# Optimization experiments

Hardware: AMD Instinct MI355X
Metric: run time of the kernel (lower is better)

## Reference

```python
import jax, jax.numpy as jnp
import numpy as np

DIM = 1024
HEADS = 16
DIM_HEAD = 64
INNER = HEADS * DIM_HEAD  # 1024
SCALE = 1.0 / DIM_HEAD ** 0.5


def setup_inputs() -> dict:
    key = jax.random.key(0)
    ks = jax.random.split(key, 5)
    x = jax.random.normal(ks[0], (4, 2048, DIM), dtype=jnp.float32)
    # nn.Linear weights stored as [out, in]; we keep [in, out] for x @ W
    Wq = jax.random.normal(ks[1], (DIM, INNER), dtype=jnp.float32) * (1.0 / np.sqrt(DIM))
    Wkv = jax.random.normal(ks[2], (DIM, 2 * INNER), dtype=jnp.float32) * (1.0 / np.sqrt(DIM))
    Wo = jax.random.normal(ks[3], (INNER, DIM), dtype=jnp.float32) * (1.0 / np.sqrt(INNER))
    bo = jax.random.normal(ks[4], (DIM,), dtype=jnp.float32) * 0.01
    return {"x": x, "Wq": Wq, "Wkv": Wkv, "Wo": Wo, "bo": bo}


def reference(x, Wq, Wkv, Wo, bo):
    b, n, _ = x.shape
    q = x @ Wq                      # [b, n, inner]
    kv = x @ Wkv                    # [b, n, 2*inner]
    k, v = jnp.split(kv, 2, axis=2)
    # 'b n (h d) -> b h n d'
    q = q.reshape(b, n, HEADS, DIM_HEAD).transpose(0, 2, 1, 3)
    k = k.reshape(b, n, HEADS, DIM_HEAD).transpose(0, 2, 1, 3)
    v = v.reshape(b, n, HEADS, DIM_HEAD).transpose(0, 2, 1, 3)
    scores = jnp.einsum('bhid,bhjd->bhij', q, k) * SCALE  # [b,h,n,n]
    attn = jax.nn.softmax(scores, axis=-1)
    out = jnp.einsum('bhij,bhjd->bhid', attn, v)          # [b,h,n,d]
    out = out.transpose(0, 2, 1, 3).reshape(b, n, INNER)  # 'b h n d -> b n (h d)'
    return out @ Wo + bo
```

## Files before the change

kernel.cpp:

```cpp
#include <hip/hip_runtime.h>
#include <hip/hip_bf16.h>

typedef unsigned short u16;
typedef unsigned int u32;
typedef __attribute__((ext_vector_type(8))) short s8v;
typedef __attribute__((ext_vector_type(4))) float f4v;
typedef __attribute__((ext_vector_type(4))) unsigned short u16x4;
typedef __attribute__((ext_vector_type(4))) unsigned int u32x4;

#define MFMA16(a,b,c) __builtin_amdgcn_mfma_f32_16x16x32_bf16((a),(b),(c),0,0,0)

#define TOKENS 8192
#define SEQ    2048
#define NH     16
#define DH     64
#define DIMK   1024
#define QPRE   0.18033688f

#if defined(__has_builtin)
#if __has_builtin(__builtin_amdgcn_exp2f)
#define EXP2(x) __builtin_amdgcn_exp2f(x)
#else
#define EXP2(x) __expf((x) * 0.69314718f)
#endif
#else
#define EXP2(x) __expf((x) * 0.69314718f)
#endif

__device__ __forceinline__ u16 f2bf(float x){
  union { float f; u32 u; } v; v.f = x;
  u32 r = v.u + 0x7FFFu + ((v.u >> 16) & 1u);
  return (u16)(r >> 16);
}

__device__ __forceinline__ void gld16(const u16* g, u16* s){
  __builtin_amdgcn_global_load_lds(
      (const __attribute__((address_space(1))) unsigned int*)(const void*)g,
      (__attribute__((address_space(3))) unsigned int*)(void*)s,
      16, 0, 0);
}

__global__ __launch_bounds__(256) void k_cast(const float* __restrict__ src,
                                              u16* __restrict__ dst){
  int i = (blockIdx.x * 256 + threadIdx.x) * 4;
  float4 v = *(const float4*)(src + i);
  u16x4 vh;
  float a[4] = {v.x, v.y, v.z, v.w};
#pragma unroll
  for (int j = 0; j < 4; j++) vh[j] = f2bf(a[j]);
  *(u16x4*)(dst + i) = vh;
}

__global__ __launch_bounds__(256) void k_transpose(const float* __restrict__ s0, int c0,
                                                   const float* __restrict__ s1, int c1,
                                                   int K, u16* __restrict__ dh){
  __shared__ float tile[64][65];
  int nb = blockIdx.x * 64, kb = blockIdx.y * 64;
  int tr = threadIdx.x >> 6, tc = threadIdx.x & 63;
#pragma unroll
  for (int i = 0; i < 16; i++){
    int k = kb + tr + i * 4, n = nb + tc;
    float v = (n < c0) ? s0[(size_t)k * c0 + n] : s1[(size_t)k * c1 + (n - c0)];
    tile[tr + i * 4][tc] = v;
  }
  __syncthreads();
#pragma unroll
  for (int i = 0; i < 16; i++){
    int nl = tr + i * 4, kl = tc;
    dh[(size_t)(nb + nl) * K + (kb + kl)] = f2bf(tile[kl][nl]);
  }
}

#define GQ_STAGE_A(buf,h,t) do{ \
  gld16(As + (size_t)(h)*131072 + (size_t)(t)*64,      &lds[(buf)*32768 + (h)*8192 + w*512]); \
  gld16(As + (size_t)(h)*131072 + (size_t)(t)*64 + 32, &lds[(buf)*32768 + (h)*8192 + 4096 + w*512]); }while(0)
#define GQ_STAGE_B(buf,h,t) do{ \
  gld16(Bs + (size_t)(h)*131072 + (size_t)(t)*64,      &lds[(buf)*32768 + 16384 + (h)*8192 + w*512]); \
  gld16(Bs + (size_t)(h)*131072 + (size_t)(t)*64 + 32, &lds[(buf)*32768 + 16384 + (h)*8192 + 4096 + w*512]); }while(0)
#define GQ_RDA(dst,buf,mh) do{ _Pragma("unroll") for (int i_ = 0; i_ < 4; i_++){ \
  dst[i_][0] = *(const s8v*)&lds[(buf)*32768 + aRB + ((mh)*4+i_)*512]; \
  dst[i_][1] = *(const s8v*)&lds[(buf)*32768 + aRB + 4096 + ((mh)*4+i_)*512]; } }while(0)
#define GQ_RDB(dst,buf,nh) do{ _Pragma("unroll") for (int j_ = 0; j_ < 2; j_++){ \
  dst[j_][0] = *(const s8v*)&lds[(buf)*32768 + bRB + ((nh)*2+j_)*512]; \
  dst[j_][1] = *(const s8v*)&lds[(buf)*32768 + bRB + 4096 + ((nh)*2+j_)*512]; } }while(0)
#define GQ_MMA(aS,bS,mh,nh) do{ __builtin_amdgcn_s_setprio(1); \
  _Pragma("unroll") for (int i_ = 0; i_ < 4; i_++) \
  _Pragma("unroll") for (int j_ = 0; j_ < 2; j_++){ \
    acc[(mh)*4+i_][(nh)*2+j_] = MFMA16(aS[i_][0], bS[j_][0], acc[(mh)*4+i_][(nh)*2+j_]); \
    acc[(mh)*4+i_][(nh)*2+j_] = MFMA16(aS[i_][1], bS[j_][1], acc[(mh)*4+i_][(nh)*2+j_]); } \
  __builtin_amdgcn_s_setprio(0); }while(0)
#define GQ_BAR() do{ asm volatile("" ::: "memory"); __builtin_amdgcn_s_barrier(); asm volatile("" ::: "memory"); }while(0)
#define GQ_VMW2() asm volatile("s_waitcnt vmcnt(2)" ::: "memory")

__global__ __launch_bounds__(512, 2) void k_gemm_qkv(
    const u16* __restrict__ A, const u16* __restrict__ B,
    u16* __restrict__ Qh, u16* __restrict__ Kh, u16* __restrict__ Vth)
{
  __shared__ u16 lds[65536];
  const int tid = threadIdx.x;
  const int w = tid >> 6, lane = tid & 63;
  const int lm = lane & 15, quad = lane >> 4;
  const int wm = w >> 2, wn = w & 3;

  const int bid = blockIdx.x;
  const int xcd = bid & 7, slot = bid >> 3;
  const int nt = slot >> 2;
  const int mloc = slot & 3;
  const int m0 = (xcd * 4 + mloc) * 256, n0 = nt * 256;

  const int srow = lane >> 2;
  const int scol = ((lane & 3) ^ (((lane >> 5) & 1) << 1)) * 8;
  const u16* As = A + (size_t)(m0 + w * 16 + srow) * DIMK + scol;
  const u16* Bs = B + (size_t)(n0 + w * 16 + srow) * DIMK + scol;

  const int swz = (lm & 8) << 1;
  const int aRB = wm * 8192 + lm * 32 + ((quad * 8) ^ swz);
  const int bRB = 16384 + (wn >> 1) * 8192 + (wn & 1) * 2048 + lm * 32 + ((quad * 8) ^ swz);

  f4v acc[8][4];
#pragma unroll
  for (int i = 0; i < 8; i++)
#pragma unroll
    for (int j = 0; j < 4; j++) acc[i][j] = (f4v){0.f, 0.f, 0.f, 0.f};

  s8v aA[4][2], aB[4][2], bA[2][2], bB[2][2];

  GQ_STAGE_A(0,0,0); GQ_STAGE_A(0,1,0); GQ_STAGE_B(0,0,0); GQ_STAGE_B(0,1,0);
  GQ_STAGE_A(1,0,1);
  GQ_VMW2(); GQ_BAR();
  GQ_RDA(aA,0,0); GQ_RDB(bA,0,0);

  for (int it = 0; it < 8; it++){
    const int t1 = 2 * it + 1;
    const int t2 = (it < 7) ? 2 * it + 2 : 15;
    const int t3 = (it < 7) ? 2 * it + 3 : 15;
    GQ_STAGE_A(1,1,t1); GQ_BAR(); GQ_RDA(aB,0,1);                 GQ_MMA(aA,bA,0,0);
    GQ_STAGE_B(1,0,t1); GQ_BAR(); GQ_RDB(bB,0,1);                 GQ_MMA(aB,bA,1,0);
    GQ_STAGE_B(1,1,t1); GQ_BAR();                                 GQ_MMA(aB,bB,1,1);
    GQ_STAGE_A(0,0,t2); GQ_VMW2(); GQ_BAR();
                                  GQ_RDA(aB,1,0); GQ_RDB(bA,1,0); GQ_MMA(aA,bB,0,1);
    GQ_STAGE_A(0,1,t2); GQ_BAR(); GQ_RDA(aA,1,1);                 GQ_MMA(aB,bA,0,0);
    GQ_STAGE_B(0,0,t2); GQ_BAR(); GQ_RDB(bB,1,1);                 GQ_MMA(aA,bA,1,0);
    GQ_STAGE_B(0,1,t2); GQ_BAR();                                 GQ_MMA(aA,bB,1,1);
    GQ_STAGE_A(1,0,t3); GQ_VMW2(); GQ_BAR();
                                  GQ_RDA(aA,0,0); GQ_RDB(bA,0,0); GQ_MMA(aB,bB,0,1);
  }

  if (nt < 8){
#pragma unroll
    for (int ig = 0; ig < 8; ig++)
#pragma unroll
      for (int jg = 0; jg < 4; jg++){
        const int gn = n0 + wn * 64 + jg * 16 + lm;
#pragma unroll
        for (int r = 0; r < 4; r++){
          const int gm = m0 + wm * 128 + ig * 16 + quad * 4 + r;
          float v = acc[ig][jg][r];
          if (gn < 1024){
            Qh[(size_t)gm * DIMK + gn] = f2bf(v * QPRE);
          } else {
            Kh[(size_t)gm * DIMK + (gn - 1024)] = f2bf(v);
          }
        }
      }
  } else {
    __syncthreads();
    u32* bnc = (u32*)lds;
#pragma unroll
    for (int igp = 0; igp < 4; igp++)
#pragma unroll
      for (int jg = 0; jg < 4; jg++){
        const int ddl = wn * 64 + jg * 16 + lm;
        const int colb = (wm * 2 + (igp >> 1)) * 32 + (igp & 1) * 16 + quad * 4;
        u32x4 p;
        p[0] = ((u32)f2bf(acc[2 * igp][jg][1])     << 16) | (u32)f2bf(acc[2 * igp][jg][0]);
        p[1] = ((u32)f2bf(acc[2 * igp][jg][3])     << 16) | (u32)f2bf(acc[2 * igp][jg][2]);
        p[2] = ((u32)f2bf(acc[2 * igp + 1][jg][1]) << 16) | (u32)f2bf(acc[2 * igp + 1][jg][0]);
        p[3] = ((u32)f2bf(acc[2 * igp + 1][jg][3]) << 16) | (u32)f2bf(acc[2 * igp + 1][jg][2]);
        const int col = colb ^ ((lm & 7) << 2);
        *(u32x4*)&bnc[ddl * 128 + col] = p;
      }
    __syncthreads();
    const int row = tid >> 1, half = tid & 1;
    const int df = n0 - 2048 + row;
    const int hh = df >> 6, dd = df & 63;
    const int bbat = m0 >> 11, ii0 = m0 & 2047;
    u32* Vg = (u32*)(Vth + ((size_t)(bbat * NH + hh) * DH + dd) * SEQ + ii0);
#pragma unroll
    for (int c = 0; c < 16; c++){
      const int cc = half * 16 + c;
      const int cb = (cc * 4) ^ ((row & 7) << 2);
      u32x4 q = *(const u32x4*)&bnc[row * 128 + cb];
      *(u32x4*)&Vg[cc * 4] = q;
    }
  }
}

__global__ __launch_bounds__(256) void k_gemm_op(
    const u16* __restrict__ A, const u16* __restrict__ B,
    const float* __restrict__ bias, float* __restrict__ Cf)
{
  __shared__ u16 sA[2][64*32], sB[2][128*32];
  const int tid = threadIdx.x, wave = tid >> 6, lane = tid & 63;
  const int lm = lane & 15, quad = lane >> 4;

  const int bid = blockIdx.x;
  const int xcd = bid & 7, slot = bid >> 3;
  const int nt = slot >> 4, mloc = slot & 15;
  const int m0 = (xcd * 16 + mloc) * 64, n0 = nt * 128;

  const int cof = (lane & 3) * 8;
  const int rsub = lane >> 2;

  f4v acc[2][4];
#pragma unroll
  for (int i = 0; i < 2; i++)
#pragma unroll
    for (int j = 0; j < 4; j++) acc[i][j] = (f4v){0.f, 0.f, 0.f, 0.f};

  const int wm = (wave >> 1) * 32, wn = (wave & 1) * 64;

  for (int kc = 0; kc < 16; kc++){
    int k = kc * 64;
#pragma unroll
    for (int cc = 0; cc < 2; cc++){
      gld16(A + (size_t)(m0 + wave * 16 + rsub) * DIMK + k + cc * 32 + cof, &sA[cc][wave * 512]);
#pragma unroll
      for (int h = 0; h < 2; h++)
        gld16(B + (size_t)(n0 + h * 64 + wave * 16 + rsub) * DIMK + k + cc * 32 + cof,
              &sB[cc][h * 2048 + wave * 512]);
    }
    __syncthreads();

#pragma unroll
    for (int cc = 0; cc < 2; cc++){
      s8v ah[2], bh[4];
#pragma unroll
      for (int i = 0; i < 2; i++)
        ah[i] = *(const s8v*)&sA[cc][(wm + i * 16 + lm) * 32 + quad * 8];
#pragma unroll
      for (int j = 0; j < 4; j++)
        bh[j] = *(const s8v*)&sB[cc][(wn + j * 16 + lm) * 32 + quad * 8];
#pragma unroll
      for (int i = 0; i < 2; i++)
#pragma unroll
        for (int j = 0; j < 4; j++)
          acc[i][j] = MFMA16(ah[i], bh[j], acc[i][j]);
    }
    __syncthreads();
  }

#pragma unroll
  for (int i = 0; i < 2; i++)
#pragma unroll
    for (int j = 0; j < 4; j++){
      int gn = n0 + wn + j * 16 + lm;
      float bv = bias[gn];
#pragma unroll
      for (int r = 0; r < 4; r++){
        int gm = m0 + wm + i * 16 + quad * 4 + r;
        Cf[(size_t)gm * DIMK + gn] = acc[i][j][r] + bv;
      }
    }
}

__global__ __launch_bounds__(256, 2) void k_attn(
    const u16* __restrict__ Qh, const u16* __restrict__ Kh, const u16* __restrict__ Vth,
    u16* __restrict__ Oh)
{
  __shared__ u16 sK[2*4096];
  __shared__ u16 sV[2*4096];

  const int bid = blockIdx.x;
  const int xcd = bid & 7, slot = bid >> 3;
  const int g = xcd * 8 + (slot >> 3);
  const int qt = slot & 7;
  const int b = g >> 4, h = g & 15;

  const int tid = threadIdx.x, wave = tid >> 6, lane = tid & 63;
  const int lm = lane & 15, quad = lane >> 4;
  const int tok0 = b * SEQ + qt * 256;
  const int rsub = lane >> 2;
  const int scof = ((lane & 3) ^ (((lane >> 5) & 1) << 1)) * 8;
  const int rsw = (lm & 8) << 1;

  s8v qf[2][4];
#pragma unroll
  for (int c = 0; c < 2; c++)
#pragma unroll
    for (int ifr = 0; ifr < 4; ifr++){
      size_t ga = (size_t)(tok0 + wave * 64 + ifr * 16 + lm) * DIMK + h * DH + c * 32 + quad * 8;
      qf[c][ifr] = *(const s8v*)(Qh + ga);
    }

  const f4v fz = (f4v){0.f, 0.f, 0.f, 0.f};

  s8v ones;
#pragma unroll
  for (int j = 0; j < 8; j++) ones[j] = (short)0x3F80;

  f4v oacc[4][4];
  f4v lacc[4];
#pragma unroll
  for (int ifr = 0; ifr < 4; ifr++){
    lacc[ifr] = (f4v){0.f, 0.f, 0.f, 0.f};
#pragma unroll
    for (int fd = 0; fd < 4; fd++) oacc[ifr][fd] = (f4v){0.f, 0.f, 0.f, 0.f};
  }

#define AT_STAGE(p, t) do{ const int jb_ = (t) * 64; \
  _Pragma("unroll") for (int c_ = 0; c_ < 2; c_++){ \
    gld16(Kh + (size_t)(b * SEQ + jb_ + wave * 16 + rsub) * DIMK + h * DH + c_ * 32 + scof, \
          &sK[(p) * 4096 + c_ * 2048 + wave * 512]); \
    gld16(Vth + (size_t)((b * NH + h) * DH + wave * 16 + rsub) * SEQ + jb_ + c_ * 32 + scof, \
          &sV[(p) * 4096 + c_ * 2048 + wave * 512]); } }while(0)
#define AT_BAR() do{ asm volatile("" ::: "memory"); __builtin_amdgcn_s_barrier(); asm volatile("" ::: "memory"); }while(0)

  AT_STAGE(0, 0);

  for (int kt = 0; kt < 32; kt++){
    const int p = kt & 1;
    AT_STAGE(p ^ 1, (kt < 31) ? (kt + 1) : 31);
    asm volatile("s_waitcnt vmcnt(4)" ::: "memory");
    AT_BAR();
    const int pb = p * 4096;

    s8v kh[2][4];
#pragma unroll
    for (int fn = 0; fn < 4; fn++){
      kh[0][fn] = *(const s8v*)&sK[pb + (fn * 16 + lm) * 32 + ((quad * 8) ^ rsw)];
      kh[1][fn] = *(const s8v*)&sK[pb + 2048 + (fn * 16 + lm) * 32 + ((quad * 8) ^ rsw)];
    }

    s8v pa[4][2];
#pragma unroll
    for (int ifr = 0; ifr < 4; ifr++){
      f4v st[4];
      __builtin_amdgcn_s_setprio(1);
#pragma unroll
      for (int fn = 0; fn < 4; fn++){
        st[fn] = MFMA16(kh[0][fn], qf[0][ifr], fz);
        st[fn] = MFMA16(kh[1][fn], qf[1][ifr], st[fn]);
      }
      __builtin_amdgcn_s_setprio(0);
#pragma unroll
      for (int fn = 0; fn < 4; fn++)
#pragma unroll
        for (int r = 0; r < 4; r++)
          st[fn][r] = EXP2(st[fn][r]);
#pragma unroll
      for (int c = 0; c < 2; c++){
        union { u32x4 w; s8v v; } u;
#pragma unroll
        for (int w2 = 0; w2 < 4; w2++){
          const int fn = c * 2 + (w2 >> 1);
          const int rr = (w2 & 1) * 2;
          union { float f; u32 u; } a0, a1;
          a0.f = st[fn][rr]; a1.f = st[fn][rr + 1];
          u.w[w2] = __builtin_amdgcn_perm(a1.u, a0.u, 0x07060302);
        }
        pa[ifr][c] = u.v;
      }
    }

    s8v vreg[2][4];
#pragma unroll
    for (int c = 0; c < 2; c++)
#pragma unroll
      for (int fd = 0; fd < 4; fd++)
        vreg[c][fd] = *(const s8v*)&sV[pb + c * 2048 + (fd * 16 + lm) * 32 + ((quad * 8) ^ rsw)];

    __builtin_amdgcn_s_setprio(1);
#pragma unroll
    for (int c = 0; c < 2; c++)
#pragma unroll
      for (int ifr = 0; ifr < 4; ifr++){
#pragma unroll
        for (int fd = 0; fd < 4; fd++)
          oacc[ifr][fd] = MFMA16(pa[ifr][c], vreg[c][fd], oacc[ifr][fd]);
        lacc[ifr] = MFMA16(pa[ifr][c], ones, lacc[ifr]);
      }
    __builtin_amdgcn_s_setprio(0);
    AT_BAR();
  }

#pragma unroll
  for (int ifr = 0; ifr < 4; ifr++){
    float inv[4];
#pragma unroll
    for (int r = 0; r < 4; r++) inv[r] = 1.f / lacc[ifr][r];
#pragma unroll
    for (int fd = 0; fd < 4; fd++){
      int dcol = h * DH + fd * 16 + lm;
#pragma unroll
      for (int r = 0; r < 4; r++){
        int tok = tok0 + wave * 64 + ifr * 16 + quad * 4 + r;
        Oh[(size_t)tok * DIMK + dcol] = f2bf(oacc[ifr][fd][r] * inv[r]);
      }
    }
  }
}

extern "C" void kernel_launch(void* const* d_in, const int* in_sizes, int n_in,
                              void* d_out, int out_size, void* d_ws, size_t ws_size,
                              hipStream_t stream) {
  const float* x   = (const float*)d_in[0];
  const float* Wq  = (const float*)d_in[1];
  const float* Wkv = (const float*)d_in[2];
  const float* Wo  = (const float*)d_in[3];
  const float* bo  = (const float*)d_in[4];
  float* out = (float*)d_out;

  char* ws = (char*)d_ws;
  size_t off = 0;
  auto alloc = [&](size_t bytes) -> u16* {
    u16* p = (u16*)(ws + off);
    off += (bytes + 255) & ~(size_t)255;
    return p;
  };
  const size_t TK2 = (size_t)TOKENS * DIMK * 2;
  u16* xh  = alloc(TK2);
  u16* Wh  = alloc((size_t)3072 * DIMK * 2);
  u16* WOh = alloc((size_t)1024 * DIMK * 2);
  u16* Qh  = alloc(TK2);
  u16* Kh  = alloc(TK2);
  u16* Vth = alloc(TK2);
  u16* Oh  = alloc(TK2);

  k_cast<<<dim3((TOKENS * DIMK) / 1024), 256, 0, stream>>>(x, xh);
  k_transpose<<<dim3(48, 16), 256, 0, stream>>>(Wq, 1024, Wkv, 2048, DIMK, Wh);
  k_transpose<<<dim3(16, 16), 256, 0, stream>>>(Wo, 1024, Wo, 1024, DIMK, WOh);
  k_gemm_qkv<<<dim3(384), 512, 0, stream>>>(xh, Wh, Qh, Kh, Vth);
  k_attn<<<dim3(512), 256, 0, stream>>>(Qh, Kh, Vth, Oh);
  k_gemm_op<<<dim3(1024), 256, 0, stream>>>(Oh, WOh, bo, out);
}
```

Before: 267.6 us.

## Double-buffer output projection GEMM with swizzled LDS and reorder QKV tile schedule

The output-projection GEMM now prefetches the next K-slice into a second LDS buffer while computing on the current one, using partial vmcnt waits and raw barriers in place of two __syncthreads per iteration. LDS reads and global-to-LDS writes use an XOR swizzle to cut bank conflicts, and MFMA sections raise wave priority. The QKV GEMM also rotates its N-tile order so the V tiles, which have the costlier transposed store, are scheduled first. The cost is doubled LDS for the projection kernel and a redundant final prefetch on the last iteration.

```diff
diff --git a/kernel.cpp b/kernel.cpp
--- a/kernel.cpp
+++ b/kernel.cpp
@@ -104,8 +104,9 @@
 
   const int bid = blockIdx.x;
   const int xcd = bid & 7, slot = bid >> 3;
-  const int nt = slot >> 2;
+  const int ntr = slot >> 2;
   const int mloc = slot & 3;
+  const int nt = (ntr < 4) ? ntr + 8 : ntr - 4;
   const int m0 = (xcd * 4 + mloc) * 256, n0 = nt * 256;
 
   const int srow = lane >> 2;
@@ -200,7 +201,8 @@
     const u16* __restrict__ A, const u16* __restrict__ B,
     const float* __restrict__ bias, float* __restrict__ Cf)
 {
-  __shared__ u16 sA[2][64*32], sB[2][128*32];
+  __shared__ u16 sA[2][4096];
+  __shared__ u16 sB[2][8192];
   const int tid = threadIdx.x, wave = tid >> 6, lane = tid & 63;
   const int lm = lane & 15, quad = lane >> 4;
 
@@ -209,8 +211,9 @@
   const int nt = slot >> 4, mloc = slot & 15;
   const int m0 = (xcd * 16 + mloc) * 64, n0 = nt * 128;
 
-  const int cof = (lane & 3) * 8;
   const int rsub = lane >> 2;
+  const int scof = ((lane & 3) ^ (((lane >> 5) & 1) << 1)) * 8;
+  const int rsw = (lm & 8) << 1;
 
   f4v acc[2][4];
 #pragma unroll
@@ -220,34 +223,42 @@
 
   const int wm = (wave >> 1) * 32, wn = (wave & 1) * 64;
 
+#define OP_STAGE(p, t) do{ const int k_ = (t) * 64; \
+  _Pragma("unroll") for (int cc_ = 0; cc_ < 2; cc_++){ \
+    gld16(A + (size_t)(m0 + wave * 16 + rsub) * DIMK + k_ + cc_ * 32 + scof, \
+          &sA[p][cc_ * 2048 + wave * 512]); \
+    _Pragma("unroll") for (int h_ = 0; h_ < 2; h_++) \
+      gld16(B + (size_t)(n0 + h_ * 64 + wave * 16 + rsub) * DIMK + k_ + cc_ * 32 + scof, \
+            &sB[p][cc_ * 4096 + h_ * 2048 + wave * 512]); \
+  } }while(0)
+#define OP_BAR() do{ asm volatile("" ::: "memory"); __builtin_amdgcn_s_barrier(); asm volatile("" ::: "memory"); }while(0)
+
+  OP_STAGE(0, 0);
+
   for (int kc = 0; kc < 16; kc++){
-    int k = kc * 64;
-#pragma unroll
-    for (int cc = 0; cc < 2; cc++){
-      gld16(A + (size_t)(m0 + wave * 16 + rsub) * DIMK + k + cc * 32 + cof, &sA[cc][wave * 512]);
-#pragma unroll
-      for (int h = 0; h < 2; h++)
-        gld16(B + (size_t)(n0 + h * 64 + wave * 16 + rsub) * DIMK + k + cc * 32 + cof,
-              &sB[cc][h * 2048 + wave * 512]);
-    }
-    __syncthreads();
+    const int p = kc & 1;
+    OP_STAGE(p ^ 1, (kc < 15) ? (kc + 1) : 15);
+    asm volatile("s_waitcnt vmcnt(6)" ::: "memory");
+    OP_BAR();
 
 #pragma unroll
     for (int cc = 0; cc < 2; cc++){
       s8v ah[2], bh[4];
 #pragma unroll
       for (int i = 0; i < 2; i++)
-        ah[i] = *(const s8v*)&sA[cc][(wm + i * 16 + lm) * 32 + quad * 8];
+        ah[i] = *(const s8v*)&sA[p][cc * 2048 + (wm + i * 16 + lm) * 32 + ((quad * 8) ^ rsw)];
 #pragma unroll
       for (int j = 0; j < 4; j++)
-        bh[j] = *(const s8v*)&sB[cc][(wn + j * 16 + lm) * 32 + quad * 8];
+        bh[j] = *(const s8v*)&sB[p][cc * 4096 + (wn + j * 16 + lm) * 32 + ((quad * 8) ^ rsw)];
+      __builtin_amdgcn_s_setprio(1);
 #pragma unroll
       for (int i = 0; i < 2; i++)
 #pragma unroll
         for (int j = 0; j < 4; j++)
           acc[i][j] = MFMA16(ah[i], bh[j], acc[i][j]);
-    }
-    __syncthreads();
+      __builtin_amdgcn_s_setprio(0);
+    }
+    OP_BAR();
   }
 
 #pragma unroll
```

New measurement: 271.8 us. About the same (+1.6%).

## Replace double-buffered QKV GEMM pipeline with single-buffer loop and reorder tiles

Applied to the files above, without the earlier changes.

The QKV projection GEMM loses its hand-scheduled double-buffered LDS pipeline, with staged loads, partial waits and barriers interleaved with MFMA groups. In its place is a simple single-buffer loop: load a K tile, sync, read fragments, run all MFMAs, sync. LDS use is halved, so the V-transpose epilogue now runs in two passes. Block-to-N-tile mapping is rotated so the V tiles, with their heavier epilogue, are scheduled first. The simpler loop loses overlap of global loads with compute, in exchange for lower LDS footprint and possibly higher occupancy.

```diff
diff --git a/kernel.cpp b/kernel.cpp
--- a/kernel.cpp
+++ b/kernel.cpp
@@ -71,32 +71,30 @@
   }
 }
 
-#define GQ_STAGE_A(buf,h,t) do{ \
-  gld16(As + (size_t)(h)*131072 + (size_t)(t)*64,      &lds[(buf)*32768 + (h)*8192 + w*512]); \
-  gld16(As + (size_t)(h)*131072 + (size_t)(t)*64 + 32, &lds[(buf)*32768 + (h)*8192 + 4096 + w*512]); }while(0)
-#define GQ_STAGE_B(buf,h,t) do{ \
-  gld16(Bs + (size_t)(h)*131072 + (size_t)(t)*64,      &lds[(buf)*32768 + 16384 + (h)*8192 + w*512]); \
-  gld16(Bs + (size_t)(h)*131072 + (size_t)(t)*64 + 32, &lds[(buf)*32768 + 16384 + (h)*8192 + 4096 + w*512]); }while(0)
-#define GQ_RDA(dst,buf,mh) do{ _Pragma("unroll") for (int i_ = 0; i_ < 4; i_++){ \
-  dst[i_][0] = *(const s8v*)&lds[(buf)*32768 + aRB + ((mh)*4+i_)*512]; \
-  dst[i_][1] = *(const s8v*)&lds[(buf)*32768 + aRB + 4096 + ((mh)*4+i_)*512]; } }while(0)
-#define GQ_RDB(dst,buf,nh) do{ _Pragma("unroll") for (int j_ = 0; j_ < 2; j_++){ \
-  dst[j_][0] = *(const s8v*)&lds[(buf)*32768 + bRB + ((nh)*2+j_)*512]; \
-  dst[j_][1] = *(const s8v*)&lds[(buf)*32768 + bRB + 4096 + ((nh)*2+j_)*512]; } }while(0)
+#define GQ_STAGE_A(h,t) do{ \
+  gld16(As + (size_t)(h)*131072 + (size_t)(t)*64,      &lds[(h)*8192 + w*512]); \
+  gld16(As + (size_t)(h)*131072 + (size_t)(t)*64 + 32, &lds[(h)*8192 + 4096 + w*512]); }while(0)
+#define GQ_STAGE_B(h,t) do{ \
+  gld16(Bs + (size_t)(h)*131072 + (size_t)(t)*64,      &lds[16384 + (h)*8192 + w*512]); \
+  gld16(Bs + (size_t)(h)*131072 + (size_t)(t)*64 + 32, &lds[16384 + (h)*8192 + 4096 + w*512]); }while(0)
+#define GQ_RDA(dst,mh) do{ _Pragma("unroll") for (int i_ = 0; i_ < 4; i_++){ \
+  dst[i_][0] = *(const s8v*)&lds[aRB + ((mh)*4+i_)*512]; \
+  dst[i_][1] = *(const s8v*)&lds[aRB + 4096 + ((mh)*4+i_)*512]; } }while(0)
+#define GQ_RDB(dst,nh) do{ _Pragma("unroll") for (int j_ = 0; j_ < 2; j_++){ \
+  dst[j_][0] = *(const s8v*)&lds[bRB + ((nh)*2+j_)*512]; \
+  dst[j_][1] = *(const s8v*)&lds[bRB + 4096 + ((nh)*2+j_)*512]; } }while(0)
 #define GQ_MMA(aS,bS,mh,nh) do{ __builtin_amdgcn_s_setprio(1); \
   _Pragma("unroll") for (int i_ = 0; i_ < 4; i_++) \
   _Pragma("unroll") for (int j_ = 0; j_ < 2; j_++){ \
     acc[(mh)*4+i_][(nh)*2+j_] = MFMA16(aS[i_][0], bS[j_][0], acc[(mh)*4+i_][(nh)*2+j_]); \
     acc[(mh)*4+i_][(nh)*2+j_] = MFMA16(aS[i_][1], bS[j_][1], acc[(mh)*4+i_][(nh)*2+j_]); } \
   __builtin_amdgcn_s_setprio(0); }while(0)
-#define GQ_BAR() do{ asm volatile("" ::: "memory"); __builtin_amdgcn_s_barrier(); asm volatile("" ::: "memory"); }while(0)
-#define GQ_VMW2() asm volatile("s_waitcnt vmcnt(2)" ::: "memory")
 
 __global__ __launch_bounds__(512, 2) void k_gemm_qkv(
     const u16* __restrict__ A, const u16* __restrict__ B,
     u16* __restrict__ Qh, u16* __restrict__ Kh, u16* __restrict__ Vth)
 {
-  __shared__ u16 lds[65536];
+  __shared__ u16 lds[32768];
   const int tid = threadIdx.x;
   const int w = tid >> 6, lane = tid & 63;
   const int lm = lane & 15, quad = lane >> 4;
@@ -104,8 +102,9 @@
 
   const int bid = blockIdx.x;
   const int xcd = bid & 7, slot = bid >> 3;
-  const int nt = slot >> 2;
+  const int ntr = slot >> 2;
   const int mloc = slot & 3;
+  const int nt = (ntr < 4) ? ntr + 8 : ntr - 4;
   const int m0 = (xcd * 4 + mloc) * 256, n0 = nt * 256;
 
   const int srow = lane >> 2;
@@ -125,25 +124,15 @@
 
   s8v aA[4][2], aB[4][2], bA[2][2], bB[2][2];
 
-  GQ_STAGE_A(0,0,0); GQ_STAGE_A(0,1,0); GQ_STAGE_B(0,0,0); GQ_STAGE_B(0,1,0);
-  GQ_STAGE_A(1,0,1);
-  GQ_VMW2(); GQ_BAR();
-  GQ_RDA(aA,0,0); GQ_RDB(bA,0,0);
-
-  for (int it = 0; it < 8; it++){
-    const int t1 = 2 * it + 1;
-    const int t2 = (it < 7) ? 2 * it + 2 : 15;
-    const int t3 = (it < 7) ? 2 * it + 3 : 15;
-    GQ_STAGE_A(1,1,t1); GQ_BAR(); GQ_RDA(aB,0,1);                 GQ_MMA(aA,bA,0,0);
-    GQ_STAGE_B(1,0,t1); GQ_BAR(); GQ_RDB(bB,0,1);                 GQ_MMA(aB,bA,1,0);
-    GQ_STAGE_B(1,1,t1); GQ_BAR();                                 GQ_MMA(aB,bB,1,1);
-    GQ_STAGE_A(0,0,t2); GQ_VMW2(); GQ_BAR();
-                                  GQ_RDA(aB,1,0); GQ_RDB(bA,1,0); GQ_MMA(aA,bB,0,1);
-    GQ_STAGE_A(0,1,t2); GQ_BAR(); GQ_RDA(aA,1,1);                 GQ_MMA(aB,bA,0,0);
-    GQ_STAGE_B(0,0,t2); GQ_BAR(); GQ_RDB(bB,1,1);                 GQ_MMA(aA,bA,1,0);
-    GQ_STAGE_B(0,1,t2); GQ_BAR();                                 GQ_MMA(aA,bB,1,1);
-    GQ_STAGE_A(1,0,t3); GQ_VMW2(); GQ_BAR();
-                                  GQ_RDA(aA,0,0); GQ_RDB(bA,0,0); GQ_MMA(aB,bB,0,1);
+  for (int kt = 0; kt < 16; kt++){
+    GQ_STAGE_A(0, kt); GQ_STAGE_A(1, kt);
+    GQ_STAGE_B(0, kt); GQ_STAGE_B(1, kt);
+    __syncthreads();
+    GQ_RDA(aA, 0); GQ_RDA(aB, 1);
+    GQ_RDB(bA, 0); GQ_RDB(bB, 1);
+    GQ_MMA(aA, bA, 0, 0); GQ_MMA(aA, bB, 0, 1);
+    GQ_MMA(aB, bA, 1, 0); GQ_MMA(aB, bB, 1, 1);
+    __syncthreads();
   }
 
   if (nt < 8){
@@ -164,34 +153,39 @@
         }
       }
   } else {
-    __syncthreads();
     u32* bnc = (u32*)lds;
 #pragma unroll
-    for (int igp = 0; igp < 4; igp++)
-#pragma unroll
-      for (int jg = 0; jg < 4; jg++){
-        const int ddl = wn * 64 + jg * 16 + lm;
-        const int colb = (wm * 2 + (igp >> 1)) * 32 + (igp & 1) * 16 + quad * 4;
-        u32x4 p;
-        p[0] = ((u32)f2bf(acc[2 * igp][jg][1])     << 16) | (u32)f2bf(acc[2 * igp][jg][0]);
-        p[1] = ((u32)f2bf(acc[2 * igp][jg][3])     << 16) | (u32)f2bf(acc[2 * igp][jg][2]);
-        p[2] = ((u32)f2bf(acc[2 * igp + 1][jg][1]) << 16) | (u32)f2bf(acc[2 * igp + 1][jg][0]);
-        p[3] = ((u32)f2bf(acc[2 * igp + 1][jg][3]) << 16) | (u32)f2bf(acc[2 * igp + 1][jg][2]);
-        const int col = colb ^ ((lm & 7) << 2);
-        *(u32x4*)&bnc[ddl * 128 + col] = p;
-      }
-    __syncthreads();
-    const int row = tid >> 1, half = tid & 1;
-    const int df = n0 - 2048 + row;
-    const int hh = df >> 6, dd = df & 63;
-    const int bbat = m0 >> 11, ii0 = m0 & 2047;
-    u32* Vg = (u32*)(Vth + ((size_t)(bbat * NH + hh) * DH + dd) * SEQ + ii0);
-#pragma unroll
-    for (int c = 0; c < 16; c++){
-      const int cc = half * 16 + c;
-      const int cb = (cc * 4) ^ ((row & 7) << 2);
-      u32x4 q = *(const u32x4*)&bnc[row * 128 + cb];
-      *(u32x4*)&Vg[cc * 4] = q;
+    for (int pass = 0; pass < 2; pass++){
+      __syncthreads();
+      if ((wn >> 1) == pass){
+#pragma unroll
+        for (int igp = 0; igp < 4; igp++)
+#pragma unroll
+          for (int jg = 0; jg < 4; jg++){
+            const int ddl = (wn & 1) * 64 + jg * 16 + lm;
+            const int colb = (wm * 2 + (igp >> 1)) * 32 + (igp & 1) * 16 + quad * 4;
+            u32x4 p;
+            p[0] = ((u32)f2bf(acc[2 * igp][jg][1])     << 16) | (u32)f2bf(acc[2 * igp][jg][0]);
+            p[1] = ((u32)f2bf(acc[2 * igp][jg][3])     << 16) | (u32)f2bf(acc[2 * igp][jg][2]);
+            p[2] = ((u32)f2bf(acc[2 * igp + 1][jg][1]) << 16) | (u32)f2bf(acc[2 * igp + 1][jg][0]);
+            p[3] = ((u32)f2bf(acc[2 * igp + 1][jg][3]) << 16) | (u32)f2bf(acc[2 * igp + 1][jg][2]);
+            const int col = colb ^ ((lm & 7) << 2);
+            *(u32x4*)&bnc[ddl * 128 + col] = p;
+          }
+      }
+      __syncthreads();
+      const int rowl = tid >> 2, qtr = tid & 3;
+      const int df = n0 - 2048 + pass * 128 + rowl;
+      const int hh = df >> 6, dd = df & 63;
+      const int bbat = m0 >> 11, ii0 = m0 & 2047;
+      u32* Vg = (u32*)(Vth + ((size_t)(bbat * NH + hh) * DH + dd) * SEQ + ii0);
+#pragma unroll
+      for (int c = 0; c < 8; c++){
+        const int cc = qtr * 8 + c;
+        const int cb = (cc * 4) ^ ((rowl & 7) << 2);
+        u32x4 q = *(const u32x4*)&bnc[rowl * 128 + cb];
+        *(u32x4*)&Vg[cc * 4] = q;
+      }
     }
   }
 }
```

After: 275.7 us. 3.0% more time.
